# Optimization experiments

Measured on AMD Instinct MI355X. Metric: run time of the kernel, lower is better.

Reference implementation:

```python
import jax, jax.numpy as jnp
import numpy as np

N_CELL = 100_000
N_NET = 100_000
N_PIN = 500_000
N_NN = 200_000
N_PAIR = 500_000
RC, RN, RP = 16, 16, 8   # raw cell/net/pin feats
HC, HN, HP = 64, 64, 8   # hidden cell/net/pin feats


def _seg(x, idx, n):
    return jax.ops.segment_sum(x, idx, num_segments=n)


def _ssp(x):  # DGL ShiftedSoftplus used inside CFConv
    return jax.nn.softplus(x) - jnp.log(2.0)


def _graph_conv(x_src, src, dst, n_src, n_dst, W, b):
    # DGL GraphConv, norm='both': c_src = out_deg^-1/2, c_dst = in_deg^-1/2, degrees clamped to >=1
    ones = jnp.ones(src.shape[0], x_src.dtype)
    cs = jnp.clip(_seg(ones, src, n_src), 1.0) ** -0.5
    cd = jnp.clip(_seg(ones, dst, n_dst), 1.0) ** -0.5
    msg = _seg((x_src * cs[:, None])[src], dst, n_dst) * cd[:, None]
    return msg @ W + b


def setup_inputs() -> dict:
    key = jax.random.key(0)
    ks = jax.random.split(key, 40)
    f = lambda i, s: jax.random.normal(ks[i], s, jnp.float32)
    p = lambda i, s: jax.random.normal(ks[i], s, jnp.float32) * 0.05
    ri = lambda i, s, hi: jax.random.randint(ks[i], s, 0, hi)
    return dict(
        cell_feat=f(0, (N_CELL, RC)),
        net_feat=f(1, (N_NET, RN)),
        pin_feat=f(2, (N_PIN, RP)),
        cell_lin_w=p(3, (RC, HC)), cell_lin_b=p(4, (HC,)),
        net_lin_w=p(5, (RN, HN)), net_lin_b=p(6, (HN,)),
        pin_lin_w=p(7, (RP, HP)), pin_lin_b=p(8, (HP,)),
        pins_w=p(9, (HC, HN)), pins_b=p(10, (HN,)),
        father_w=p(11, (HN, HN)), father_b=p(12, (HN,)),
        son_w=p(13, (HN, HN)), son_b=p(14, (HN,)),
        cf_node_w=p(15, (HN, HC)), cf_node_b=p(16, (HC,)),
        cf_e1_w=p(17, (RP, HC)), cf_e1_b=p(18, (HC,)),
        cf_e2_w=p(19, (HC, HC)), cf_e2_b=p(20, (HC,)),
        cf_out_w=p(21, (HC, HC)), cf_out_b=p(22, (HC,)),
        net_dis_w=p(23, (2 * HN, 1)), net_dis_b=p(24, (1,)),
        net_angle_w=p(25, (2 * HN, 1)), net_angle_b=p(26, (1,)),
        pin_dis_w=p(27, (HC + HP + HN, 1)), pin_dis_b=p(28, (1,)),
        pin_angle_w=p(29, (HC + HP + HN, 1)), pin_angle_b=p(30, (1,)),
        pin_net=ri(31, (N_PIN,), N_NET),
        pin_cell=ri(32, (N_PIN,), N_CELL),
        nn_src=ri(33, (N_NN,), N_NET),
        nn_dst=ri(34, (N_NN,), N_NET),
        net_net_pairs=ri(35, (N_PAIR, 2), N_NET),
    )


def reference(cell_feat, net_feat, pin_feat,
              cell_lin_w, cell_lin_b, net_lin_w, net_lin_b, pin_lin_w, pin_lin_b,
              pins_w, pins_b, father_w, father_b, son_w, son_b,
              cf_node_w, cf_node_b, cf_e1_w, cf_e1_b, cf_e2_w, cf_e2_b, cf_out_w, cf_out_b,
              net_dis_w, net_dis_b, net_angle_w, net_angle_b,
              pin_dis_w, pin_dis_b, pin_angle_w, pin_angle_b,
              pin_net, pin_cell, nn_src, nn_dst, net_net_pairs):
    h_cell = jnp.tanh(cell_feat @ cell_lin_w + cell_lin_b)
    h_net = jnp.tanh(net_feat @ net_lin_w + net_lin_b)
    h_pin = jnp.tanh(pin_feat @ pin_lin_w + pin_lin_b)

    # HeteroGraphConv with aggregate='max' (all relations read the PRE-update h)
    net_pins = _graph_conv(h_cell, pin_cell, pin_net, N_CELL, N_NET, pins_w, pins_b)   # cell->net
    net_fa = _graph_conv(h_net, nn_src, nn_dst, N_NET, N_NET, father_w, father_b)      # net->net
    net_so = _graph_conv(h_net, nn_dst, nn_src, N_NET, N_NET, son_w, son_b)            # reversed
    h_net2 = jnp.maximum(jnp.maximum(net_pins, net_fa), net_so)

    # CFConv net->cell; NOTE: original passes RAW pin_feat as edge feats
    e = _ssp(_ssp(pin_feat @ cf_e1_w + cf_e1_b) @ cf_e2_w + cf_e2_b)   # [P, HC]
    hv = h_net @ cf_node_w + cf_node_b                                  # [Nn, HC]
    h_cell2 = _ssp(_seg(hv[pin_net] * e, pin_cell, N_CELL) @ cf_out_w + cf_out_b)

    # gather-based pairwise readouts
    npair = jnp.concatenate([h_net2[net_net_pairs[:, 0]], h_net2[net_net_pairs[:, 1]]], axis=-1)
    npc = jnp.concatenate([h_net2[pin_net], h_pin, h_cell2[pin_cell]], axis=-1)
    net_dis = jax.nn.softplus(npair @ net_dis_w + net_dis_b)[:, 0]
    net_angle = (npair @ net_angle_w + net_angle_b)[:, 0]
    pin_dis = jax.nn.softplus(npc @ pin_dis_w + pin_dis_b)[:, 0]
    pin_angle = (npc @ pin_angle_w + pin_angle_b)[:, 0]
    return (net_dis, net_angle, pin_dis, pin_angle)
```

## Files before the change

### kernel.cpp

```cpp
#include <hip/hip_runtime.h>
#include <math.h>

#define NCELL 100000
#define NNET  100000
#define NPIN  500000
#define NNN   200000
#define NPAIR 500000
#define NSCAN (4 * NNET)
#define SCAN_BLOCKS ((NSCAN + 1023) / 1024)
#define PART_SZ ((NNET + 7) / 8)

#define GA_DEG 1024
#define GA_LIN 1024
#define GB_EMLP 1024
#define GB_HV   256
#define GB_GP   384
#define GB_GFS  384

typedef __attribute__((ext_vector_type(8))) short short8;
typedef __attribute__((ext_vector_type(4))) float f32x4;
typedef unsigned short u16;
typedef unsigned int u32;
typedef unsigned long long u64;

__device__ __forceinline__ u16 f2bf(float x) {
    union { float f; u32 u; } v; v.f = x;
    u32 r = (v.u + 0x7FFF + ((v.u >> 16) & 1)) >> 16;
    return (u16)r;
}
__device__ __forceinline__ float bf2f(u16 u) {
    union { u32 u; float f; } v; v.u = ((u32)u) << 16; return v.f;
}
__device__ __forceinline__ u32 cvtpk(float lo, float hi) {
    u32 r;
    asm("v_cvt_pk_bf16_f32 %0, %1, %2" : "=v"(r) : "v"(lo), "v"(hi));
    return r;
}
__device__ __forceinline__ u16 f2bf_fast(float v) {
    return (u16)(cvtpk(v, v) & 0xffffu);
}
__device__ __forceinline__ float plo(u32 h) { return bf2f((u16)(h & 0xffff)); }
__device__ __forceinline__ float phi(u32 h) { return bf2f((u16)(h >> 16)); }

__device__ __forceinline__ float softplusf(float x) {
    return fmaxf(x, 0.f) + __logf(1.f + __expf(-fabsf(x)));
}
__device__ __forceinline__ float sspf(float x) {
    return softplusf(x) - 0.69314718055994530942f;
}
__device__ __forceinline__ float ftanh(float x) {
    float xc = fminf(fmaxf(x, -9.f), 9.f);
    float e = __expf(2.f * xc);
    return (e - 1.f) * __builtin_amdgcn_rcpf(e + 1.f);
}

__device__ __forceinline__ short8 load_bfrag(const float* __restrict__ W,
                                             int kt, int nt, int lane) {
    int k0 = kt * 32 + ((lane >> 4) & 3) * 8;
    int c = nt * 16 + (lane & 15);
    short8 f;
#pragma unroll
    for (int j = 0; j < 8; j++) f[j] = (short)f2bf(W[(k0 + j) * 64 + c]);
    return f;
}

__global__ __launch_bounds__(256) void k_fusedA(
    const int* __restrict__ pin_cell, const int* __restrict__ pin_net,
    const int* __restrict__ nn_src, const int* __restrict__ nn_dst,
    u32* __restrict__ cnt,
    u32* __restrict__ rankNp, u32* __restrict__ rankC,
    u32* __restrict__ rankD, u32* __restrict__ rankS,
    const float* __restrict__ cf, const float* __restrict__ nf,
    const float* __restrict__ Wc, const float* __restrict__ bc,
    const float* __restrict__ Wn, const float* __restrict__ bn,
    u16* __restrict__ h_cell, u16* __restrict__ h_net) {
    if (blockIdx.x < GA_DEG) {
        int stride = GA_DEG * 256;
        for (int i = blockIdx.x * 256 + threadIdx.x; i < NPIN; i += stride) {
            rankNp[i] = atomicAdd(&cnt[pin_net[i]], 1u);
            rankC[i]  = atomicAdd(&cnt[NNET + pin_cell[i]], 1u);
        }
        for (int i = blockIdx.x * 256 + threadIdx.x; i < NNN; i += stride) {
            rankD[i] = atomicAdd(&cnt[2 * NNET + nn_dst[i]], 1u);
            rankS[i] = atomicAdd(&cnt[3 * NNET + nn_src[i]], 1u);
        }
    } else {
        int tid = threadIdx.x, lane = tid & 63, w = tid >> 6;
        float wc[16], wn[16];
#pragma unroll
        for (int k = 0; k < 16; k++) { wc[k] = Wc[k * 64 + lane]; wn[k] = Wn[k * 64 + lane]; }
        float bC = bc[lane], bN = bn[lane];
        int wave = (blockIdx.x - GA_DEG) * 4 + w, nw = GA_LIN * 4;
        for (int r = wave; r < NCELL; r += nw) {
            const float4* ip = (const float4*)(cf + (size_t)r * 16);
            float4 a = ip[0], bv = ip[1], c = ip[2], d = ip[3];
            float acc = bC;
            acc = fmaf(a.x, wc[0], acc);  acc = fmaf(a.y, wc[1], acc);
            acc = fmaf(a.z, wc[2], acc);  acc = fmaf(a.w, wc[3], acc);
            acc = fmaf(bv.x, wc[4], acc); acc = fmaf(bv.y, wc[5], acc);
            acc = fmaf(bv.z, wc[6], acc); acc = fmaf(bv.w, wc[7], acc);
            acc = fmaf(c.x, wc[8], acc);  acc = fmaf(c.y, wc[9], acc);
            acc = fmaf(c.z, wc[10], acc); acc = fmaf(c.w, wc[11], acc);
            acc = fmaf(d.x, wc[12], acc); acc = fmaf(d.y, wc[13], acc);
            acc = fmaf(d.z, wc[14], acc); acc = fmaf(d.w, wc[15], acc);
            float v = ftanh(acc);
            float vp = __shfl_xor(v, 1, 64);
            if (!(lane & 1))
                *(u32*)(h_cell + (size_t)r * 64 + lane) = cvtpk(v, vp);
        }
        for (int r = wave; r < NNET; r += nw) {
            const float4* ip = (const float4*)(nf + (size_t)r * 16);
            float4 a = ip[0], bv = ip[1], c = ip[2], d = ip[3];
            float acc = bN;
            acc = fmaf(a.x, wn[0], acc);  acc = fmaf(a.y, wn[1], acc);
            acc = fmaf(a.z, wn[2], acc);  acc = fmaf(a.w, wn[3], acc);
            acc = fmaf(bv.x, wn[4], acc); acc = fmaf(bv.y, wn[5], acc);
            acc = fmaf(bv.z, wn[6], acc); acc = fmaf(bv.w, wn[7], acc);
            acc = fmaf(c.x, wn[8], acc);  acc = fmaf(c.y, wn[9], acc);
            acc = fmaf(c.z, wn[10], acc); acc = fmaf(c.w, wn[11], acc);
            acc = fmaf(d.x, wn[12], acc); acc = fmaf(d.y, wn[13], acc);
            acc = fmaf(d.z, wn[14], acc); acc = fmaf(d.w, wn[15], acc);
            float v = ftanh(acc);
            float vp = __shfl_xor(v, 1, 64);
            if (!(lane & 1))
                *(u32*)(h_net + (size_t)r * 64 + lane) = cvtpk(v, vp);
        }
    }
}

__global__ __launch_bounds__(256) void k_scan1(const u32* __restrict__ in,
                                               u32* __restrict__ out, u32* __restrict__ bsum,
                                               float* __restrict__ deg) {
    __shared__ u32 sc[256];
    int t = threadIdx.x;
    int base = blockIdx.x * 1024 + t * 4;
    u32 v0 = base + 0 < NSCAN ? in[base + 0] : 0;
    u32 v1 = base + 1 < NSCAN ? in[base + 1] : 0;
    u32 v2 = base + 2 < NSCAN ? in[base + 2] : 0;
    u32 v3 = base + 3 < NSCAN ? in[base + 3] : 0;
    if (base + 0 < NSCAN) deg[base + 0] = rsqrtf((float)max(v0, 1u));
    if (base + 1 < NSCAN) deg[base + 1] = rsqrtf((float)max(v1, 1u));
    if (base + 2 < NSCAN) deg[base + 2] = rsqrtf((float)max(v2, 1u));
    if (base + 3 < NSCAN) deg[base + 3] = rsqrtf((float)max(v3, 1u));
    u32 s = v0 + v1 + v2 + v3;
    sc[t] = s; __syncthreads();
    for (int off = 1; off < 256; off <<= 1) {
        u32 x = (t >= off) ? sc[t - off] : 0; __syncthreads();
        sc[t] += x; __syncthreads();
    }
    u32 excl = sc[t] - s;
    if (base + 0 < NSCAN) out[base + 0] = excl;
    if (base + 1 < NSCAN) out[base + 1] = excl + v0;
    if (base + 2 < NSCAN) out[base + 2] = excl + v0 + v1;
    if (base + 3 < NSCAN) out[base + 3] = excl + v0 + v1 + v2;
    if (t == 255) bsum[blockIdx.x] = sc[255];
}

__global__ __launch_bounds__(512) void k_scan2(u32* __restrict__ bsum) {
    __shared__ u32 sc[512];
    int t = threadIdx.x;
    u32 v = (t < SCAN_BLOCKS) ? bsum[t] : 0;
    sc[t] = v; __syncthreads();
    for (int off = 1; off < 512; off <<= 1) {
        u32 x = (t >= off) ? sc[t - off] : 0; __syncthreads();
        sc[t] += x; __syncthreads();
    }
    if (t < SCAN_BLOCKS) bsum[t] = sc[t] - v;
}

__global__ __launch_bounds__(256) void k_scan3(u32* __restrict__ S, const u32* __restrict__ bsum) {
    int i = blockIdx.x * blockDim.x + threadIdx.x;
    if (i < NSCAN) S[i] = S[i] + bsum[i >> 10];
    if (i == 0) S[NSCAN] = 2u * NPIN + 2u * NNN;
}

__global__ __launch_bounds__(256) void k_place_part(
    const int* __restrict__ pin_cell, const int* __restrict__ pin_net,
    const int* __restrict__ nn_src, const int* __restrict__ nn_dst,
    const u32* __restrict__ S,
    const u32* __restrict__ rankNp, const u32* __restrict__ rankC,
    const u32* __restrict__ rankD, const u32* __restrict__ rankS,
    u32* __restrict__ colC, u64* __restrict__ colPN,
    u32* __restrict__ colS, u32* __restrict__ colD) {
    int part = blockIdx.x & 7;
    int grp = blockIdx.x >> 3;
    int ngrp = gridDim.x >> 3;
    int lo = part * PART_SZ, hi = lo + PART_SZ;
    int stride = ngrp * 256;
    for (int e = grp * 256 + threadIdx.x; e < NPIN; e += stride) {
        int n = pin_net[e], c = pin_cell[e];
        if (n >= lo && n < hi)
            colC[S[n] + rankNp[e]] = (u32)c;
        if (c >= lo && c < hi)
            colPN[S[NNET + c] + rankC[e] - NPIN] = (u64)(u32)e | ((u64)(u32)n << 32);
    }
    for (int i = grp * 256 + threadIdx.x; i < NNN; i += stride) {
        int s = nn_src[i], d = nn_dst[i];
        if (d >= lo && d < hi)
            colS[S[2 * NNET + d] + rankD[i] - 2u * NPIN] = (u32)s;
        if (s >= lo && s < hi)
            colD[S[3 * NNET + s] + rankS[i] - (2u * NPIN + NNN)] = (u32)d;
    }
}

__global__ __launch_bounds__(256, 4) void k_fusedB(
    const float* __restrict__ pin_feat, const u64* __restrict__ colPN,
    const float* __restrict__ E1, const float* __restrict__ b1,
    const float* __restrict__ E2, const float* __restrict__ b2,
    u16* __restrict__ etab,
    const u16* __restrict__ h_net, const float* __restrict__ Whv,
    const float* __restrict__ bhv, u16* __restrict__ hv,
    const u32* __restrict__ S, const u32* __restrict__ colC,
    const u16* __restrict__ h_cell, const float* __restrict__ rCv,
    u16* __restrict__ accP,
    const u32* __restrict__ colS, const u32* __restrict__ colD,
    const float* __restrict__ rDv, const float* __restrict__ rSv,
    u16* __restrict__ accF, u16* __restrict__ accS) {
    __shared__ __align__(16) u16 sm[4][1024];
    int tid = threadIdx.x, lane = tid & 63, w = tid >> 6;
    int l15 = lane & 15, g = (lane >> 4) & 3;
    f32x4 z = {0.f, 0.f, 0.f, 0.f};
    if (blockIdx.x < GB_EMLP) {
        short8 B1[4];
#pragma unroll
        for (int nt = 0; nt < 4; nt++) {
            short8 f = {0, 0, 0, 0, 0, 0, 0, 0};
            if (lane < 16) {
                int c = nt * 16 + l15;
#pragma unroll
                for (int j = 0; j < 8; j++) f[j] = (short)f2bf(E1[j * 64 + c]);
            }
            B1[nt] = f;
        }
        short8 B2[2][4];
#pragma unroll
        for (int kt = 0; kt < 2; kt++)
#pragma unroll
            for (int nt = 0; nt < 4; nt++) B2[kt][nt] = load_bfrag(E2, kt, nt, lane);
        float bb1[4], bb2[4];
#pragma unroll
        for (int nt = 0; nt < 4; nt++) {
            bb1[nt] = b1[nt * 16 + l15];
            bb2[nt] = b2[nt * 16 + l15];
        }
        int wave = blockIdx.x * 4 + w, nwave = GB_EMLP * 4;
        const int ntile = NPIN >> 4;
        for (int t = wave; t < ntile; t += nwave) {
            int P = t << 4;
            short8 a1 = {0, 0, 0, 0, 0, 0, 0, 0};
            if (lane < 16) {
                u32 p = (u32)colPN[P + lane];
                const float4* q = (const float4*)(pin_feat + (size_t)p * 8);
                float4 u0 = q[0], u1 = q[1];
                u32 w01 = cvtpk(u0.x, u0.y), w23 = cvtpk(u0.z, u0.w);
                u32 w45 = cvtpk(u1.x, u1.y), w67 = cvtpk(u1.z, u1.w);
                a1[0] = (short)(w01 & 0xffff); a1[1] = (short)(w01 >> 16);
                a1[2] = (short)(w23 & 0xffff); a1[3] = (short)(w23 >> 16);
                a1[4] = (short)(w45 & 0xffff); a1[5] = (short)(w45 >> 16);
                a1[6] = (short)(w67 & 0xffff); a1[7] = (short)(w67 >> 16);
            }
#pragma unroll
            for (int nt = 0; nt < 4; nt++) {
                f32x4 c1 = __builtin_amdgcn_mfma_f32_16x16x32_bf16(a1, B1[nt], z, 0, 0, 0);
#pragma unroll
                for (int r = 0; r < 4; r++) {
                    int row = g * 4 + r;
                    int col = nt * 16 + l15;
                    sm[w][row * 64 + (col ^ ((row & 7) << 3))] = f2bf_fast(sspf(c1[r] + bb1[nt]));
                }
            }
            short8 a2[2];
#pragma unroll
            for (int kt = 0; kt < 2; kt++) {
                int idx = l15 * 64 + ((kt * 32 + g * 8) ^ ((l15 & 7) << 3));
                a2[kt] = *(const short8*)&sm[w][idx];
            }
#pragma unroll
            for (int nt = 0; nt < 4; nt++) {
                f32x4 e = __builtin_amdgcn_mfma_f32_16x16x32_bf16(a2[0], B2[0][nt], z, 0, 0, 0);
                e = __builtin_amdgcn_mfma_f32_16x16x32_bf16(a2[1], B2[1][nt], e, 0, 0, 0);
#pragma unroll
                for (int r = 0; r < 4; r++) {
                    float v = sspf(e[r] + bb2[nt]);
                    float vp = __shfl_xor(v, 1, 64);
                    if (!(lane & 1))
                        *(u32*)(etab + (size_t)(P + g * 4 + r) * 64 + nt * 16 + l15) = cvtpk(v, vp);
                }
            }
        }
    } else if (blockIdx.x < GB_EMLP + GB_HV) {
        short8 Bf[2][4];
        float bias[4];
#pragma unroll
        for (int kt = 0; kt < 2; kt++)
#pragma unroll
            for (int nt = 0; nt < 4; nt++) Bf[kt][nt] = load_bfrag(Whv, kt, nt, lane);
#pragma unroll
        for (int nt = 0; nt < 4; nt++) bias[nt] = bhv[nt * 16 + l15];
        int wave = (blockIdx.x - GB_EMLP) * 4 + w, nwave = GB_HV * 4;
        int ntile = NNET >> 4;
        for (int t = wave; t < ntile; t += nwave) {
            int R = t << 4;
            const u16* rb = h_net + (size_t)(R + l15) * 64;
            short8 a0 = *(const short8*)(rb + g * 8);
            short8 a1 = *(const short8*)(rb + 32 + g * 8);
#pragma unroll
            for (int nt = 0; nt < 4; nt++) {
                f32x4 acc = __builtin_amdgcn_mfma_f32_16x16x32_bf16(a0, Bf[0][nt], z, 0, 0, 0);
                acc = __builtin_amdgcn_mfma_f32_16x16x32_bf16(a1, Bf[1][nt], acc, 0, 0, 0);
#pragma unroll
                for (int r = 0; r < 4; r++) {
                    float v = acc[r] + bias[nt];
                    float vp = __shfl_xor(v, 1, 64);
                    if (!(lane & 1))
                        *(u32*)(hv + (size_t)(R + g * 4 + r) * 64 + nt * 16 + l15) = cvtpk(v, vp);
                }
            }
        }
    } else if (blockIdx.x < GB_EMLP + GB_HV + GB_GP) {
        int l32 = tid & 31, off2 = l32 * 2;
        int slot = (blockIdx.x - GB_EMLP - GB_HV) * 8 + (tid >> 5), ns = GB_GP * 8;
        for (int n = slot; n < NNET; n += ns) {
            u32 b0 = S[n], b1 = S[n + 1];
            float fa = 0.f, fb = 0.f, ga = 0.f, gb = 0.f;
            u32 k = b0;
            for (; k + 1 < b1; k += 2) {
                u32 c0 = colC[k], c1 = colC[k + 1];
                float r0 = rCv[c0], r1 = rCv[c1];
                u32 h0 = *(const u32*)(h_cell + (size_t)c0 * 64 + off2);
                u32 h1 = *(const u32*)(h_cell + (size_t)c1 * 64 + off2);
                fa = fmaf(plo(h0), r0, fa); fb = fmaf(phi(h0), r0, fb);
                ga = fmaf(plo(h1), r1, ga); gb = fmaf(phi(h1), r1, gb);
            }
            if (k < b1) {
                u32 c0 = colC[k];
                float r0 = rCv[c0];
                u32 h0 = *(const u32*)(h_cell + (size_t)c0 * 64 + off2);
                fa = fmaf(plo(h0), r0, fa); fb = fmaf(phi(h0), r0, fb);
            }
            *(u32*)(accP + (size_t)n * 64 + off2) = cvtpk(fa + ga, fb + gb);
        }
    } else {
        int l32 = tid & 31, off2 = l32 * 2;
        int slot = (blockIdx.x - GB_EMLP - GB_HV - GB_GP) * 8 + (tid >> 5), ns = GB_GFS * 8;
        for (int r = slot; r < 2 * NNET; r += ns) {
            if (r < NNET) {
                int d = r;
                u32 b0 = S[2 * NNET + d] - 2u * NPIN, b1 = S[2 * NNET + d + 1] - 2u * NPIN;
                float fa = 0.f, fb = 0.f, ga = 0.f, gb = 0.f;
                u32 k = b0;
                for (; k + 1 < b1; k += 2) {
                    u32 s0 = colS[k], s1 = colS[k + 1];
                    float c0 = rSv[s0], c1 = rSv[s1];
                    u32 h0 = *(const u32*)(h_net + (size_t)s0 * 64 + off2);
                    u32 h1 = *(const u32*)(h_net + (size_t)s1 * 64 + off2);
                    fa = fmaf(plo(h0), c0, fa); fb = fmaf(phi(h0), c0, fb);
                    ga = fmaf(plo(h1), c1, ga); gb = fmaf(phi(h1), c1, gb);
                }
                if (k < b1) {
                    u32 s0 = colS[k];
                    float c0 = rSv[s0];
                    u32 h0 = *(const u32*)(h_net + (size_t)s0 * 64 + off2);
                    fa = fmaf(plo(h0), c0, fa); fb = fmaf(phi(h0), c0, fb);
                }
                *(u32*)(accF + (size_t)d * 64 + off2) = cvtpk(fa + ga, fb + gb);
            } else {
                int s = r - NNET;
                u32 b0 = S[3 * NNET + s] - (2u * NPIN + NNN), b1 = S[3 * NNET + s + 1] - (2u * NPIN + NNN);
                float fa = 0.f, fb = 0.f, ga = 0.f, gb = 0.f;
                u32 k = b0;
                for (; k + 1 < b1; k += 2) {
                    u32 d0 = colD[k], d1 = colD[k + 1];
                    float c0 = rDv[d0], c1 = rDv[d1];
                    u32 h0 = *(const u32*)(h_net + (size_t)d0 * 64 + off2);
                    u32 h1 = *(const u32*)(h_net + (size_t)d1 * 64 + off2);
                    fa = fmaf(plo(h0), c0, fa); fb = fmaf(phi(h0), c0, fb);
                    ga = fmaf(plo(h1), c1, ga); gb = fmaf(phi(h1), c1, gb);
                }
                if (k < b1) {
                    u32 d0 = colD[k];
                    float c0 = rDv[d0];
                    u32 h0 = *(const u32*)(h_net + (size_t)d0 * 64 + off2);
                    fa = fmaf(plo(h0), c0, fa); fb = fmaf(phi(h0), c0, fb);
                }
                *(u32*)(accS + (size_t)s * 64 + off2) = cvtpk(fa + ga, fb + gb);
            }
        }
    }
}

__global__ __launch_bounds__(256) void k_gatherCell(
    const u32* __restrict__ S, const u64* __restrict__ colPN,
    const u16* __restrict__ etab, const u16* __restrict__ hv, u16* __restrict__ acc) {
    int l32 = threadIdx.x & 31, off2 = l32 * 2;
    int slot = blockIdx.x * 8 + (threadIdx.x >> 5), ns = gridDim.x * 8;
    for (int c = slot; c < NCELL; c += ns) {
        u32 b0 = S[NNET + c] - NPIN, b1 = S[NNET + c + 1] - NPIN;
        float fa = 0.f, fb = 0.f, ga = 0.f, gb = 0.f;
        u32 k = b0;
        for (; k + 1 < b1; k += 2) {
            u32 n0 = (u32)(colPN[k] >> 32), n1 = (u32)(colPN[k + 1] >> 32);
            u32 e0 = *(const u32*)(etab + (size_t)k * 64 + off2);
            u32 e1 = *(const u32*)(etab + (size_t)(k + 1) * 64 + off2);
            u32 h0 = *(const u32*)(hv + (size_t)n0 * 64 + off2);
            u32 h1 = *(const u32*)(hv + (size_t)n1 * 64 + off2);
            fa = fmaf(plo(e0), plo(h0), fa); fb = fmaf(phi(e0), phi(h0), fb);
            ga = fmaf(plo(e1), plo(h1), ga); gb = fmaf(phi(e1), phi(h1), gb);
        }
        if (k < b1) {
            u32 n0 = (u32)(colPN[k] >> 32);
            u32 e0 = *(const u32*)(etab + (size_t)k * 64 + off2);
            u32 h0 = *(const u32*)(hv + (size_t)n0 * 64 + off2);
            fa = fmaf(plo(e0), plo(h0), fa); fb = fmaf(phi(e0), phi(h0), fb);
        }
        *(u32*)(acc + (size_t)c * 64 + off2) = cvtpk(fa + ga, fb + gb);
    }
}

__global__ __launch_bounds__(256, 2) void k_combine3(
    const u16* __restrict__ A0, const float* __restrict__ W0, const float* __restrict__ b0,
    const u16* __restrict__ A1, const float* __restrict__ W1, const float* __restrict__ b1,
    const u16* __restrict__ A2, const float* __restrict__ W2, const float* __restrict__ b2,
    const float* __restrict__ sc0, const float* __restrict__ sc1, const float* __restrict__ sc2,
    const float* __restrict__ ndw, const float* __restrict__ naw,
    const float* __restrict__ pdw, const float* __restrict__ paw,
    float* __restrict__ ntab, int n) {
    int tid = threadIdx.x, lane = tid & 63, w = tid >> 6;
    int l15 = lane & 15, g = (lane >> 4) & 3;
    const float* Ws[3] = {W0, W1, W2};
    const float* bs[3] = {b0, b1, b2};
    const u16* As[3] = {A0, A1, A2};
    short8 Bf[3][2][4];
    float bias[3][4];
#pragma unroll
    for (int rel = 0; rel < 3; rel++) {
#pragma unroll
        for (int kt = 0; kt < 2; kt++)
#pragma unroll
            for (int nt = 0; nt < 4; nt++) Bf[rel][kt][nt] = load_bfrag(Ws[rel], kt, nt, lane);
#pragma unroll
        for (int nt = 0; nt < 4; nt++) bias[rel][nt] = bs[rel][nt * 16 + l15];
    }
    float wt[6][4];
#pragma unroll
    for (int nt = 0; nt < 4; nt++) {
        int c = nt * 16 + l15;
        wt[0][nt] = ndw[c];      wt[1][nt] = naw[c];
        wt[2][nt] = ndw[64 + c]; wt[3][nt] = naw[64 + c];
        wt[4][nt] = pdw[c];      wt[5][nt] = paw[c];
    }
    int wave = blockIdx.x * 4 + w, nwave = gridDim.x * 4;
    int ntile = n >> 4;
    f32x4 z = {0.f, 0.f, 0.f, 0.f};
    for (int t = wave; t < ntile; t += nwave) {
        int R = t << 4;
        int rowA = R + l15;
        float s0a[4], s1a[4], s2a[4];
        *(float4*)s0a = *(const float4*)(sc0 + R + g * 4);
        *(float4*)s1a = *(const float4*)(sc1 + R + g * 4);
        *(float4*)s2a = *(const float4*)(sc2 + R + g * 4);
        f32x4 res[4];
#pragma unroll
        for (int rel = 0; rel < 3; rel++) {
            const u16* rb = As[rel] + (size_t)rowA * 64;
            short8 a0 = *(const short8*)(rb + g * 8);
            short8 a1 = *(const short8*)(rb + 32 + g * 8);
            const float* sa = (rel == 0) ? s0a : (rel == 1) ? s1a : s2a;
#pragma unroll
            for (int nt = 0; nt < 4; nt++) {
                f32x4 acc = __builtin_amdgcn_mfma_f32_16x16x32_bf16(a0, Bf[rel][0][nt], z, 0, 0, 0);
                acc = __builtin_amdgcn_mfma_f32_16x16x32_bf16(a1, Bf[rel][1][nt], acc, 0, 0, 0);
                if (rel == 0) {
#pragma unroll
                    for (int r = 0; r < 4; r++) res[nt][r] = sa[r] * acc[r] + bias[0][nt];
                } else {
#pragma unroll
                    for (int r = 0; r < 4; r++)
                        res[nt][r] = fmaxf(res[nt][r], sa[r] * acc[r] + bias[rel][nt]);
                }
            }
        }
#pragma unroll
        for (int r = 0; r < 4; r++) {
            float a0 = 0.f, a1 = 0.f, a2 = 0.f, a3 = 0.f, a4 = 0.f, a5 = 0.f;
#pragma unroll
            for (int nt = 0; nt < 4; nt++) {
                float v = res[nt][r];
                a0 = fmaf(v, wt[0][nt], a0);
                a1 = fmaf(v, wt[1][nt], a1);
                a2 = fmaf(v, wt[2][nt], a2);
                a3 = fmaf(v, wt[3][nt], a3);
                a4 = fmaf(v, wt[4][nt], a4);
                a5 = fmaf(v, wt[5][nt], a5);
            }
#pragma unroll
            for (int off = 1; off < 16; off <<= 1) {
                a0 += __shfl_xor(a0, off, 64);
                a1 += __shfl_xor(a1, off, 64);
                a2 += __shfl_xor(a2, off, 64);
                a3 += __shfl_xor(a3, off, 64);
                a4 += __shfl_xor(a4, off, 64);
                a5 += __shfl_xor(a5, off, 64);
            }
            if (l15 == 0) {
                float* tp = ntab + (size_t)(R + g * 4 + r) * 8;
                *(float2*)tp = float2{a0, a1};
                *(float2*)(tp + 2) = float2{a2, a3};
                *(float2*)(tp + 4) = float2{a4, a5};
            }
        }
    }
}

__global__ __launch_bounds__(256, 3) void k_mm64c(
    const u16* __restrict__ in, const float* __restrict__ W, const float* __restrict__ b,
    const float* __restrict__ pdw, const float* __restrict__ paw,
    float* __restrict__ ctab, int n) {
    int tid = threadIdx.x, lane = tid & 63, w = tid >> 6;
    int l15 = lane & 15, g = (lane >> 4) & 3;
    short8 Bf[2][4];
    float bias[4], wdv[4], wav[4];
#pragma unroll
    for (int kt = 0; kt < 2; kt++)
#pragma unroll
        for (int nt = 0; nt < 4; nt++) Bf[kt][nt] = load_bfrag(W, kt, nt, lane);
#pragma unroll
    for (int nt = 0; nt < 4; nt++) {
        int c = nt * 16 + l15;
        bias[nt] = b[c];
        wdv[nt] = pdw[72 + c];
        wav[nt] = paw[72 + c];
    }
    int wave = blockIdx.x * 4 + w, nwave = gridDim.x * 4;
    int ntile = n >> 4;
    f32x4 z = {0.f, 0.f, 0.f, 0.f};
    for (int t = wave; t < ntile; t += nwave) {
        int R = t << 4;
        const u16* rb = in + (size_t)(R + l15) * 64;
        short8 a0 = *(const short8*)(rb + g * 8);
        short8 a1 = *(const short8*)(rb + 32 + g * 8);
        float sd[4] = {0.f, 0.f, 0.f, 0.f}, sa[4] = {0.f, 0.f, 0.f, 0.f};
#pragma unroll
        for (int nt = 0; nt < 4; nt++) {
            f32x4 acc = __builtin_amdgcn_mfma_f32_16x16x32_bf16(a0, Bf[0][nt], z, 0, 0, 0);
            acc = __builtin_amdgcn_mfma_f32_16x16x32_bf16(a1, Bf[1][nt], acc, 0, 0, 0);
#pragma unroll
            for (int r = 0; r < 4; r++) {
                float v = sspf(acc[r] + bias[nt]);
                sd[r] = fmaf(v, wdv[nt], sd[r]);
                sa[r] = fmaf(v, wav[nt], sa[r]);
            }
        }
#pragma unroll
        for (int r = 0; r < 4; r++) {
            float d = sd[r], a = sa[r];
#pragma unroll
            for (int off = 1; off < 16; off <<= 1) {
                d += __shfl_xor(d, off, 64);
                a += __shfl_xor(a, off, 64);
            }
            if (l15 == 0)
                *(float2*)(ctab + (size_t)(R + g * 4 + r) * 2) = float2{d, a};
        }
    }
}

__global__ __launch_bounds__(256) void k_readout(
    const int* __restrict__ pairs,
    const float* __restrict__ pin_feat,
    const int* __restrict__ pin_net, const int* __restrict__ pin_cell,
    const float* __restrict__ ntab, const float* __restrict__ ctab,
    const float* __restrict__ plw, const float* __restrict__ plb,
    const float* __restrict__ pdw, const float* __restrict__ paw,
    const float* __restrict__ nbd, const float* __restrict__ nba,
    const float* __restrict__ pbd, const float* __restrict__ pba,
    float* __restrict__ out) {
    int i = blockIdx.x * blockDim.x + threadIdx.x;
    if (i < NPAIR) {
        int p0 = pairs[2 * i], p1 = pairs[2 * i + 1];
        float2 x0 = *(const float2*)(ntab + (size_t)p0 * 8);
        float2 x1 = *(const float2*)(ntab + (size_t)p1 * 8 + 2);
        out[i] = softplusf(x0.x + x1.x + nbd[0]);
        out[NPAIR + i] = x0.y + x1.y + nba[0];
    } else if (i < NPAIR + NPIN) {
        int p = i - NPAIR;
        int n = pin_net[p], c = pin_cell[p];
        float2 ns = *(const float2*)(ntab + (size_t)n * 8 + 4);
        float2 cs = *(const float2*)(ctab + (size_t)c * 2);
        float pf[8];
        *(float4*)pf = *(const float4*)(pin_feat + (size_t)p * 8);
        *(float4*)(pf + 4) = *(const float4*)(pin_feat + (size_t)p * 8 + 4);
        float sd = ns.x + cs.x + pbd[0];
        float sa = ns.y + cs.y + pba[0];
#pragma unroll
        for (int j = 0; j < 8; j++) {
            float a = plb[j];
#pragma unroll
            for (int k = 0; k < 8; k++) a = fmaf(pf[k], plw[k * 8 + j], a);
            float hp = ftanh(a);
            sd = fmaf(hp, pdw[64 + j], sd);
            sa = fmaf(hp, paw[64 + j], sa);
        }
        out[2 * NPAIR + p] = softplusf(sd);
        out[2 * NPAIR + NPIN + p] = sa;
    }
}

extern "C" void kernel_launch(void* const* d_in, const int* in_sizes, int n_in,
                              void* d_out, int out_size, void* d_ws, size_t ws_size,
                              hipStream_t stream) {
    const float* cell_feat = (const float*)d_in[0];
    const float* net_feat  = (const float*)d_in[1];
    const float* pin_feat  = (const float*)d_in[2];
    const float* cell_lin_w = (const float*)d_in[3];
    const float* cell_lin_b = (const float*)d_in[4];
    const float* net_lin_w  = (const float*)d_in[5];
    const float* net_lin_b  = (const float*)d_in[6];
    const float* pin_lin_w  = (const float*)d_in[7];
    const float* pin_lin_b  = (const float*)d_in[8];
    const float* pins_w   = (const float*)d_in[9];
    const float* pins_b   = (const float*)d_in[10];
    const float* father_w = (const float*)d_in[11];
    const float* father_b = (const float*)d_in[12];
    const float* son_w    = (const float*)d_in[13];
    const float* son_b    = (const float*)d_in[14];
    const float* cf_node_w = (const float*)d_in[15];
    const float* cf_node_b = (const float*)d_in[16];
    const float* cf_e1_w  = (const float*)d_in[17];
    const float* cf_e1_b  = (const float*)d_in[18];
    const float* cf_e2_w  = (const float*)d_in[19];
    const float* cf_e2_b  = (const float*)d_in[20];
    const float* cf_out_w = (const float*)d_in[21];
    const float* cf_out_b = (const float*)d_in[22];
    const float* net_dis_w   = (const float*)d_in[23];
    const float* net_dis_b   = (const float*)d_in[24];
    const float* net_angle_w = (const float*)d_in[25];
    const float* net_angle_b = (const float*)d_in[26];
    const float* pin_dis_w   = (const float*)d_in[27];
    const float* pin_dis_b   = (const float*)d_in[28];
    const float* pin_angle_w = (const float*)d_in[29];
    const float* pin_angle_b = (const float*)d_in[30];
    const int* pin_net = (const int*)d_in[31];
    const int* pin_cell = (const int*)d_in[32];
    const int* nn_src = (const int*)d_in[33];
    const int* nn_dst = (const int*)d_in[34];
    const int* pairs = (const int*)d_in[35];

    u16* ws16 = (u16*)d_ws;
    const size_t SZ = (size_t)NNET * 64;
    u16* h_cell   = ws16;
    u16* acc_cell = ws16;
    u16* h_net    = ws16 + SZ;
    u16* accP     = ws16 + 2 * SZ;
    u16* accF     = ws16 + 3 * SZ;
    u16* accS     = ws16 + 4 * SZ;
    u16* etab     = ws16 + 5 * SZ;
    u16* hv       = ws16 + 10 * SZ;
    u32* tail = (u32*)(ws16 + 11 * SZ);
    u32* cnt    = tail;
    u32* Sarr   = cnt + NSCAN;
    u32* rankNp = Sarr + NSCAN + 2;
    u32* rankC  = rankNp + NPIN;
    u32* rankD  = rankC + NPIN;
    u32* rankS  = rankD + NNN;
    u32* colC   = rankS + NNN;
    u32* colS   = colC + NPIN;
    u32* colD   = colS + NNN;
    u64* colPN  = (u64*)(colD + NNN);
    u32* bsum   = (u32*)(colPN + NPIN);
    float* deg  = (float*)(bsum + 512);
    float* rNp = deg;
    float* rC  = deg + NNET;
    float* rD  = deg + 2 * NNET;
    float* rS  = deg + 3 * NNET;
    float* ntab = deg + NSCAN;
    float* ctab = ntab + (size_t)NNET * 8;

    hipMemsetAsync(cnt, 0, NSCAN * sizeof(u32), stream);

    k_fusedA<<<GA_DEG + GA_LIN, 256, 0, stream>>>(
        pin_cell, pin_net, nn_src, nn_dst, cnt, rankNp, rankC, rankD, rankS,
        cell_feat, net_feat, cell_lin_w, cell_lin_b, net_lin_w, net_lin_b,
        h_cell, h_net);

    k_scan1<<<SCAN_BLOCKS, 256, 0, stream>>>(cnt, Sarr, bsum, deg);
    k_scan2<<<1, 512, 0, stream>>>(bsum);
    k_scan3<<<(NSCAN + 255) / 256, 256, 0, stream>>>(Sarr, bsum);
    k_place_part<<<2048, 256, 0, stream>>>(pin_cell, pin_net, nn_src, nn_dst,
                                           Sarr, rankNp, rankC, rankD, rankS,
                                           colC, colPN, colS, colD);

    k_fusedB<<<GB_EMLP + GB_HV + GB_GP + GB_GFS, 256, 0, stream>>>(
        pin_feat, colPN, cf_e1_w, cf_e1_b, cf_e2_w, cf_e2_b, etab,
        h_net, cf_node_w, cf_node_b, hv,
        Sarr, colC, h_cell, rC, accP,
        colS, colD, rD, rS, accF, accS);

    k_combine3<<<512, 256, 0, stream>>>(accP, pins_w, pins_b,
                                        accF, father_w, father_b,
                                        accS, son_w, son_b,
                                        rNp, rD, rS,
                                        net_dis_w, net_angle_w, pin_dis_w, pin_angle_w,
                                        ntab, NNET);

    k_gatherCell<<<2048, 256, 0, stream>>>(Sarr, colPN, etab, hv, acc_cell);

    k_mm64c<<<512, 256, 0, stream>>>(acc_cell, cf_out_w, cf_out_b,
                                     pin_dis_w, pin_angle_w, ctab, NCELL);

    float* out = (float*)d_out;
    k_readout<<<(NPAIR + NPIN + 255) / 256, 256, 0, stream>>>(
        pairs, pin_feat, pin_net, pin_cell, ntab, ctab,
        pin_lin_w, pin_lin_b, pin_dis_w, pin_angle_w,
        net_dis_b, net_angle_b, pin_dis_b, pin_angle_b, out);
}
```

Measured before the change: 341.4 us.

## Split fused heterogeneous kernel into four separate launches

The single block-partitioned kernel that ran the edge MLP, the hv matmul and three graph gathers concurrently is split into four kernels launched back to back on the same stream, each using its full grid. This drops the fixed block split between workloads, which could leave the device idle while the slowest branch finished, and lets each kernel get its own register and occupancy profile. In exchange the four phases no longer overlap, and three extra launches plus inter-kernel gaps are added.

```diff
diff --git a/kernel.cpp b/kernel.cpp
--- a/kernel.cpp
+++ b/kernel.cpp
@@ -12,10 +12,6 @@
 
 #define GA_DEG 1024
 #define GA_LIN 1024
-#define GB_EMLP 1024
-#define GB_HV   256
-#define GB_GP   384
-#define GB_GFS  384
 
 typedef __attribute__((ext_vector_type(8))) short short8;
 typedef __attribute__((ext_vector_type(4))) float f32x4;
@@ -203,188 +199,195 @@
     }
 }
 
-__global__ __launch_bounds__(256, 4) void k_fusedB(
+__global__ __launch_bounds__(256, 4) void k_emlp(
     const float* __restrict__ pin_feat, const u64* __restrict__ colPN,
     const float* __restrict__ E1, const float* __restrict__ b1,
     const float* __restrict__ E2, const float* __restrict__ b2,
-    u16* __restrict__ etab,
-    const u16* __restrict__ h_net, const float* __restrict__ Whv,
-    const float* __restrict__ bhv, u16* __restrict__ hv,
-    const u32* __restrict__ S, const u32* __restrict__ colC,
-    const u16* __restrict__ h_cell, const float* __restrict__ rCv,
-    u16* __restrict__ accP,
-    const u32* __restrict__ colS, const u32* __restrict__ colD,
-    const float* __restrict__ rDv, const float* __restrict__ rSv,
-    u16* __restrict__ accF, u16* __restrict__ accS) {
+    u16* __restrict__ etab) {
     __shared__ __align__(16) u16 sm[4][1024];
     int tid = threadIdx.x, lane = tid & 63, w = tid >> 6;
     int l15 = lane & 15, g = (lane >> 4) & 3;
+    short8 B1[4];
+#pragma unroll
+    for (int nt = 0; nt < 4; nt++) {
+        short8 f = {0, 0, 0, 0, 0, 0, 0, 0};
+        if (lane < 16) {
+            int c = nt * 16 + l15;
+#pragma unroll
+            for (int j = 0; j < 8; j++) f[j] = (short)f2bf(E1[j * 64 + c]);
+        }
+        B1[nt] = f;
+    }
+    short8 B2[2][4];
+#pragma unroll
+    for (int kt = 0; kt < 2; kt++)
+#pragma unroll
+        for (int nt = 0; nt < 4; nt++) B2[kt][nt] = load_bfrag(E2, kt, nt, lane);
+    float bb1[4], bb2[4];
+#pragma unroll
+    for (int nt = 0; nt < 4; nt++) {
+        bb1[nt] = b1[nt * 16 + l15];
+        bb2[nt] = b2[nt * 16 + l15];
+    }
+    int wave = blockIdx.x * 4 + w, nwave = gridDim.x * 4;
+    const int ntile = NPIN >> 4;
     f32x4 z = {0.f, 0.f, 0.f, 0.f};
-    if (blockIdx.x < GB_EMLP) {
-        short8 B1[4];
+    for (int t = wave; t < ntile; t += nwave) {
+        int P = t << 4;
+        short8 a1 = {0, 0, 0, 0, 0, 0, 0, 0};
+        if (lane < 16) {
+            u32 p = (u32)colPN[P + lane];
+            const float4* q = (const float4*)(pin_feat + (size_t)p * 8);
+            float4 u0 = q[0], u1 = q[1];
+            u32 w01 = cvtpk(u0.x, u0.y), w23 = cvtpk(u0.z, u0.w);
+            u32 w45 = cvtpk(u1.x, u1.y), w67 = cvtpk(u1.z, u1.w);
+            a1[0] = (short)(w01 & 0xffff); a1[1] = (short)(w01 >> 16);
+            a1[2] = (short)(w23 & 0xffff); a1[3] = (short)(w23 >> 16);
+            a1[4] = (short)(w45 & 0xffff); a1[5] = (short)(w45 >> 16);
+            a1[6] = (short)(w67 & 0xffff); a1[7] = (short)(w67 >> 16);
+        }
 #pragma unroll
         for (int nt = 0; nt < 4; nt++) {
-            short8 f = {0, 0, 0, 0, 0, 0, 0, 0};
-            if (lane < 16) {
-                int c = nt * 16 + l15;
-#pragma unroll
-                for (int j = 0; j < 8; j++) f[j] = (short)f2bf(E1[j * 64 + c]);
-            }
-            B1[nt] = f;
-        }
-        short8 B2[2][4];
-#pragma unroll
-        for (int kt = 0; kt < 2; kt++)
-#pragma unroll
-            for (int nt = 0; nt < 4; nt++) B2[kt][nt] = load_bfrag(E2, kt, nt, lane);
-        float bb1[4], bb2[4];
+            f32x4 c1 = __builtin_amdgcn_mfma_f32_16x16x32_bf16(a1, B1[nt], z, 0, 0, 0);
+#pragma unroll
+            for (int r = 0; r < 4; r++) {
+                int row = g * 4 + r;
+                int col = nt * 16 + l15;
+                sm[w][row * 64 + (col ^ ((row & 7) << 3))] = f2bf_fast(sspf(c1[r] + bb1[nt]));
+            }
+        }
+        short8 a2[2];
+#pragma unroll
+        for (int kt = 0; kt < 2; kt++) {
+            int idx = l15 * 64 + ((kt * 32 + g * 8) ^ ((l15 & 7) << 3));
+            a2[kt] = *(const short8*)&sm[w][idx];
+        }
 #pragma unroll
         for (int nt = 0; nt < 4; nt++) {
-            bb1[nt] = b1[nt * 16 + l15];
-            bb2[nt] = b2[nt * 16 + l15];
-        }
-        int wave = blockIdx.x * 4 + w, nwave = GB_EMLP * 4;
-        const int ntile = NPIN >> 4;
-        for (int t = wave; t < ntile; t += nwave) {
-            int P = t << 4;
-            short8 a1 = {0, 0, 0, 0, 0, 0, 0, 0};
-            if (lane < 16) {
-                u32 p = (u32)colPN[P + lane];
-                const float4* q = (const float4*)(pin_feat + (size_t)p * 8);
-                float4 u0 = q[0], u1 = q[1];
-                u32 w01 = cvtpk(u0.x, u0.y), w23 = cvtpk(u0.z, u0.w);
-                u32 w45 = cvtpk(u1.x, u1.y), w67 = cvtpk(u1.z, u1.w);
-                a1[0] = (short)(w01 & 0xffff); a1[1] = (short)(w01 >> 16);
-                a1[2] = (short)(w23 & 0xffff); a1[3] = (short)(w23 >> 16);
-                a1[4] = (short)(w45 & 0xffff); a1[5] = (short)(w45 >> 16);
-                a1[6] = (short)(w67 & 0xffff); a1[7] = (short)(w67 >> 16);
-            }
-#pragma unroll
-            for (int nt = 0; nt < 4; nt++) {
-                f32x4 c1 = __builtin_amdgcn_mfma_f32_16x16x32_bf16(a1, B1[nt], z, 0, 0, 0);
-#pragma unroll
-                for (int r = 0; r < 4; r++) {
-                    int row = g * 4 + r;
-                    int col = nt * 16 + l15;
-                    sm[w][row * 64 + (col ^ ((row & 7) << 3))] = f2bf_fast(sspf(c1[r] + bb1[nt]));
-                }
-            }
-            short8 a2[2];
-#pragma unroll
-            for (int kt = 0; kt < 2; kt++) {
-                int idx = l15 * 64 + ((kt * 32 + g * 8) ^ ((l15 & 7) << 3));
-                a2[kt] = *(const short8*)&sm[w][idx];
-            }
-#pragma unroll
-            for (int nt = 0; nt < 4; nt++) {
-                f32x4 e = __builtin_amdgcn_mfma_f32_16x16x32_bf16(a2[0], B2[0][nt], z, 0, 0, 0);
-                e = __builtin_amdgcn_mfma_f32_16x16x32_bf16(a2[1], B2[1][nt], e, 0, 0, 0);
-#pragma unroll
-                for (int r = 0; r < 4; r++) {
-                    float v = sspf(e[r] + bb2[nt]);
-                    float vp = __shfl_xor(v, 1, 64);
-                    if (!(lane & 1))
-                        *(u32*)(etab + (size_t)(P + g * 4 + r) * 64 + nt * 16 + l15) = cvtpk(v, vp);
-                }
-            }
-        }
-    } else if (blockIdx.x < GB_EMLP + GB_HV) {
-        short8 Bf[2][4];
-        float bias[4];
-#pragma unroll
-        for (int kt = 0; kt < 2; kt++)
-#pragma unroll
-            for (int nt = 0; nt < 4; nt++) Bf[kt][nt] = load_bfrag(Whv, kt, nt, lane);
-#pragma unroll
-        for (int nt = 0; nt < 4; nt++) bias[nt] = bhv[nt * 16 + l15];
-        int wave = (blockIdx.x - GB_EMLP) * 4 + w, nwave = GB_HV * 4;
-        int ntile = NNET >> 4;
-        for (int t = wave; t < ntile; t += nwave) {
-            int R = t << 4;
-            const u16* rb = h_net + (size_t)(R + l15) * 64;
-            short8 a0 = *(const short8*)(rb + g * 8);
-            short8 a1 = *(const short8*)(rb + 32 + g * 8);
-#pragma unroll
-            for (int nt = 0; nt < 4; nt++) {
-                f32x4 acc = __builtin_amdgcn_mfma_f32_16x16x32_bf16(a0, Bf[0][nt], z, 0, 0, 0);
-                acc = __builtin_amdgcn_mfma_f32_16x16x32_bf16(a1, Bf[1][nt], acc, 0, 0, 0);
-#pragma unroll
-                for (int r = 0; r < 4; r++) {
-                    float v = acc[r] + bias[nt];
-                    float vp = __shfl_xor(v, 1, 64);
-                    if (!(lane & 1))
-                        *(u32*)(hv + (size_t)(R + g * 4 + r) * 64 + nt * 16 + l15) = cvtpk(v, vp);
-                }
-            }
-        }
-    } else if (blockIdx.x < GB_EMLP + GB_HV + GB_GP) {
-        int l32 = tid & 31, off2 = l32 * 2;
-        int slot = (blockIdx.x - GB_EMLP - GB_HV) * 8 + (tid >> 5), ns = GB_GP * 8;
-        for (int n = slot; n < NNET; n += ns) {
-            u32 b0 = S[n], b1 = S[n + 1];
+            f32x4 e = __builtin_amdgcn_mfma_f32_16x16x32_bf16(a2[0], B2[0][nt], z, 0, 0, 0);
+            e = __builtin_amdgcn_mfma_f32_16x16x32_bf16(a2[1], B2[1][nt], e, 0, 0, 0);
+#pragma unroll
+            for (int r = 0; r < 4; r++) {
+                float v = sspf(e[r] + bb2[nt]);
+                float vp = __shfl_xor(v, 1, 64);
+                if (!(lane & 1))
+                    *(u32*)(etab + (size_t)(P + g * 4 + r) * 64 + nt * 16 + l15) = cvtpk(v, vp);
+            }
+        }
+    }
+}
+
+__global__ __launch_bounds__(256, 4) void k_mm64hv(
+    const u16* __restrict__ in, const float* __restrict__ W,
+    const float* __restrict__ b, u16* __restrict__ out, int n) {
+    int tid = threadIdx.x, lane = tid & 63, w = tid >> 6;
+    int l15 = lane & 15, g = (lane >> 4) & 3;
+    short8 Bf[2][4];
+    float bias[4];
+#pragma unroll
+    for (int kt = 0; kt < 2; kt++)
+#pragma unroll
+        for (int nt = 0; nt < 4; nt++) Bf[kt][nt] = load_bfrag(W, kt, nt, lane);
+#pragma unroll
+    for (int nt = 0; nt < 4; nt++) bias[nt] = b[nt * 16 + l15];
+    int wave = blockIdx.x * 4 + w, nwave = gridDim.x * 4;
+    int ntile = n >> 4;
+    f32x4 z = {0.f, 0.f, 0.f, 0.f};
+    for (int t = wave; t < ntile; t += nwave) {
+        int R = t << 4;
+        const u16* rb = in + (size_t)(R + l15) * 64;
+        short8 a0 = *(const short8*)(rb + g * 8);
+        short8 a1 = *(const short8*)(rb + 32 + g * 8);
+#pragma unroll
+        for (int nt = 0; nt < 4; nt++) {
+            f32x4 acc = __builtin_amdgcn_mfma_f32_16x16x32_bf16(a0, Bf[0][nt], z, 0, 0, 0);
+            acc = __builtin_amdgcn_mfma_f32_16x16x32_bf16(a1, Bf[1][nt], acc, 0, 0, 0);
+#pragma unroll
+            for (int r = 0; r < 4; r++) {
+                float v = acc[r] + bias[nt];
+                float vp = __shfl_xor(v, 1, 64);
+                if (!(lane & 1))
+                    *(u32*)(out + (size_t)(R + g * 4 + r) * 64 + nt * 16 + l15) = cvtpk(v, vp);
+            }
+        }
+    }
+}
+
+__global__ __launch_bounds__(256) void k_gatherP(
+    const u32* __restrict__ S, const u32* __restrict__ colC,
+    const u16* __restrict__ h_cell, const float* __restrict__ rCv,
+    u16* __restrict__ accP) {
+    int l32 = threadIdx.x & 31, off2 = l32 * 2;
+    int slot = blockIdx.x * 8 + (threadIdx.x >> 5), ns = gridDim.x * 8;
+    for (int n = slot; n < NNET; n += ns) {
+        u32 b0 = S[n], b1 = S[n + 1];
+        float fa = 0.f, fb = 0.f, ga = 0.f, gb = 0.f;
+        u32 k = b0;
+        for (; k + 1 < b1; k += 2) {
+            u32 c0 = colC[k], c1 = colC[k + 1];
+            float r0 = rCv[c0], r1 = rCv[c1];
+            u32 h0 = *(const u32*)(h_cell + (size_t)c0 * 64 + off2);
+            u32 h1 = *(const u32*)(h_cell + (size_t)c1 * 64 + off2);
+            fa = fmaf(plo(h0), r0, fa); fb = fmaf(phi(h0), r0, fb);
+            ga = fmaf(plo(h1), r1, ga); gb = fmaf(phi(h1), r1, gb);
+        }
+        if (k < b1) {
+            u32 c0 = colC[k];
+            float r0 = rCv[c0];
+            u32 h0 = *(const u32*)(h_cell + (size_t)c0 * 64 + off2);
+            fa = fmaf(plo(h0), r0, fa); fb = fmaf(phi(h0), r0, fb);
+        }
+        *(u32*)(accP + (size_t)n * 64 + off2) = cvtpk(fa + ga, fb + gb);
+    }
+}
+
+__global__ __launch_bounds__(256) void k_gatherFS(
+    const u32* __restrict__ S, const u32* __restrict__ colS, const u32* __restrict__ colD,
+    const u16* __restrict__ h_net, const float* __restrict__ rDv, const float* __restrict__ rSv,
+    u16* __restrict__ accF, u16* __restrict__ accS) {
+    int l32 = threadIdx.x & 31, off2 = l32 * 2;
+    int slot = blockIdx.x * 8 + (threadIdx.x >> 5), ns = gridDim.x * 8;
+    for (int r = slot; r < 2 * NNET; r += ns) {
+        if (r < NNET) {
+            int d = r;
+            u32 b0 = S[2 * NNET + d] - 2u * NPIN, b1 = S[2 * NNET + d + 1] - 2u * NPIN;
             float fa = 0.f, fb = 0.f, ga = 0.f, gb = 0.f;
             u32 k = b0;
             for (; k + 1 < b1; k += 2) {
-                u32 c0 = colC[k], c1 = colC[k + 1];
-                float r0 = rCv[c0], r1 = rCv[c1];
-                u32 h0 = *(const u32*)(h_cell + (size_t)c0 * 64 + off2);
-                u32 h1 = *(const u32*)(h_cell + (size_t)c1 * 64 + off2);
-                fa = fmaf(plo(h0), r0, fa); fb = fmaf(phi(h0), r0, fb);
-                ga = fmaf(plo(h1), r1, ga); gb = fmaf(phi(h1), r1, gb);
+                u32 s0 = colS[k], s1 = colS[k + 1];
+                float c0 = rSv[s0], c1 = rSv[s1];
+                u32 h0 = *(const u32*)(h_net + (size_t)s0 * 64 + off2);
+                u32 h1 = *(const u32*)(h_net + (size_t)s1 * 64 + off2);
+                fa = fmaf(plo(h0), c0, fa); fb = fmaf(phi(h0), c0, fb);
+                ga = fmaf(plo(h1), c1, ga); gb = fmaf(phi(h1), c1, gb);
             }
             if (k < b1) {
-                u32 c0 = colC[k];
-                float r0 = rCv[c0];
-                u32 h0 = *(const u32*)(h_cell + (size_t)c0 * 64 + off2);
-                fa = fmaf(plo(h0), r0, fa); fb = fmaf(phi(h0), r0, fb);
-            }
-            *(u32*)(accP + (size_t)n * 64 + off2) = cvtpk(fa + ga, fb + gb);
-        }
-    } else {
-        int l32 = tid & 31, off2 = l32 * 2;
-        int slot = (blockIdx.x - GB_EMLP - GB_HV - GB_GP) * 8 + (tid >> 5), ns = GB_GFS * 8;
-        for (int r = slot; r < 2 * NNET; r += ns) {
-            if (r < NNET) {
-                int d = r;
-                u32 b0 = S[2 * NNET + d] - 2u * NPIN, b1 = S[2 * NNET + d + 1] - 2u * NPIN;
-                float fa = 0.f, fb = 0.f, ga = 0.f, gb = 0.f;
-                u32 k = b0;
-                for (; k + 1 < b1; k += 2) {
-                    u32 s0 = colS[k], s1 = colS[k + 1];
-                    float c0 = rSv[s0], c1 = rSv[s1];
-                    u32 h0 = *(const u32*)(h_net + (size_t)s0 * 64 + off2);
-                    u32 h1 = *(const u32*)(h_net + (size_t)s1 * 64 + off2);
-                    fa = fmaf(plo(h0), c0, fa); fb = fmaf(phi(h0), c0, fb);
-                    ga = fmaf(plo(h1), c1, ga); gb = fmaf(phi(h1), c1, gb);
-                }
-                if (k < b1) {
-                    u32 s0 = colS[k];
-                    float c0 = rSv[s0];
-                    u32 h0 = *(const u32*)(h_net + (size_t)s0 * 64 + off2);
-                    fa = fmaf(plo(h0), c0, fa); fb = fmaf(phi(h0), c0, fb);
-                }
-                *(u32*)(accF + (size_t)d * 64 + off2) = cvtpk(fa + ga, fb + gb);
-            } else {
-                int s = r - NNET;
-                u32 b0 = S[3 * NNET + s] - (2u * NPIN + NNN), b1 = S[3 * NNET + s + 1] - (2u * NPIN + NNN);
-                float fa = 0.f, fb = 0.f, ga = 0.f, gb = 0.f;
-                u32 k = b0;
-                for (; k + 1 < b1; k += 2) {
-                    u32 d0 = colD[k], d1 = colD[k + 1];
-                    float c0 = rDv[d0], c1 = rDv[d1];
-                    u32 h0 = *(const u32*)(h_net + (size_t)d0 * 64 + off2);
-                    u32 h1 = *(const u32*)(h_net + (size_t)d1 * 64 + off2);
-                    fa = fmaf(plo(h0), c0, fa); fb = fmaf(phi(h0), c0, fb);
-                    ga = fmaf(plo(h1), c1, ga); gb = fmaf(phi(h1), c1, gb);
-                }
-                if (k < b1) {
-                    u32 d0 = colD[k];
-                    float c0 = rDv[d0];
-                    u32 h0 = *(const u32*)(h_net + (size_t)d0 * 64 + off2);
-                    fa = fmaf(plo(h0), c0, fa); fb = fmaf(phi(h0), c0, fb);
-                }
-                *(u32*)(accS + (size_t)s * 64 + off2) = cvtpk(fa + ga, fb + gb);
-            }
+                u32 s0 = colS[k];
+                float c0 = rSv[s0];
+                u32 h0 = *(const u32*)(h_net + (size_t)s0 * 64 + off2);
+                fa = fmaf(plo(h0), c0, fa); fb = fmaf(phi(h0), c0, fb);
+            }
+            *(u32*)(accF + (size_t)d * 64 + off2) = cvtpk(fa + ga, fb + gb);
+        } else {
+            int s = r - NNET;
+            u32 b0 = S[3 * NNET + s] - (2u * NPIN + NNN), b1 = S[3 * NNET + s + 1] - (2u * NPIN + NNN);
+            float fa = 0.f, fb = 0.f, ga = 0.f, gb = 0.f;
+            u32 k = b0;
+            for (; k + 1 < b1; k += 2) {
+                u32 d0 = colD[k], d1 = colD[k + 1];
+                float c0 = rDv[d0], c1 = rDv[d1];
+                u32 h0 = *(const u32*)(h_net + (size_t)d0 * 64 + off2);
+                u32 h1 = *(const u32*)(h_net + (size_t)d1 * 64 + off2);
+                fa = fmaf(plo(h0), c0, fa); fb = fmaf(phi(h0), c0, fb);
+                ga = fmaf(plo(h1), c1, ga); gb = fmaf(phi(h1), c1, gb);
+            }
+            if (k < b1) {
+                u32 d0 = colD[k];
+                float c0 = rDv[d0];
+                u32 h0 = *(const u32*)(h_net + (size_t)d0 * 64 + off2);
+                fa = fmaf(plo(h0), c0, fa); fb = fmaf(phi(h0), c0, fb);
+            }
+            *(u32*)(accS + (size_t)s * 64 + off2) = cvtpk(fa + ga, fb + gb);
         }
     }
 }
@@ -690,11 +693,10 @@
                                            Sarr, rankNp, rankC, rankD, rankS,
                                            colC, colPN, colS, colD);
 
-    k_fusedB<<<GB_EMLP + GB_HV + GB_GP + GB_GFS, 256, 0, stream>>>(
-        pin_feat, colPN, cf_e1_w, cf_e1_b, cf_e2_w, cf_e2_b, etab,
-        h_net, cf_node_w, cf_node_b, hv,
-        Sarr, colC, h_cell, rC, accP,
-        colS, colD, rD, rS, accF, accS);
+    k_emlp<<<2048, 256, 0, stream>>>(pin_feat, colPN, cf_e1_w, cf_e1_b, cf_e2_w, cf_e2_b, etab);
+    k_mm64hv<<<1024, 256, 0, stream>>>(h_net, cf_node_w, cf_node_b, hv, NNET);
+    k_gatherP<<<2048, 256, 0, stream>>>(Sarr, colC, h_cell, rC, accP);
+    k_gatherFS<<<2048, 256, 0, stream>>>(Sarr, colS, colD, h_net, rD, rS, accF, accS);
 
     k_combine3<<<512, 256, 0, stream>>>(accP, pins_w, pins_b,
                                         accF, father_w, father_b,
```

Result: faster. 301.4 us (-11.7%).
